# Optimization experiments

Measured on AMD Instinct MI355X. Metric: run time of the kernel, lower is better.

Reference implementation:

```python
import jax, jax.numpy as jnp
import numpy as np

B, S, D = 4, 512, 256
NEG = -1e30  # finite stand-in for -inf so fully-masked row 0 stays NaN-free


def setup_inputs() -> dict:
    key = jax.random.key(0)
    ks = jax.random.split(key, 10)
    s = 0.02
    return {
        "x": jax.random.normal(ks[0], (B, S, D), dtype=jnp.float32),
        # edge_mlp: Linear(3D -> D), ReLU, Linear(D -> 1). Stored [in, out].
        "W1": jax.random.normal(ks[1], (3 * D, D), dtype=jnp.float32) * s,
        "b1": jnp.zeros((D,), dtype=jnp.float32),
        "w2": jax.random.normal(ks[2], (D, 1), dtype=jnp.float32) * s,
        "b2": jnp.zeros((1,), dtype=jnp.float32),
        "Wv": jax.random.normal(ks[3], (D, D), dtype=jnp.float32) * s,
        "bv": jnp.zeros((D,), dtype=jnp.float32),
        "Wo": jax.random.normal(ks[4], (D, D), dtype=jnp.float32) * s,
        "bo": jnp.zeros((D,), dtype=jnp.float32),
        "gamma": jnp.ones((D,), dtype=jnp.float32),
        "beta": jnp.zeros((D,), dtype=jnp.float32),
    }


def reference(x, W1, b1, w2, b2, Wv, bv, Wo, bo, gamma, beta):
    b, seq, d = x.shape
    # edge_mlp layer1 on concat([x_i, x_j, x_i - x_j]) decomposes linearly:
    # h[b,i,j,:] = x_i @ (Wa + Wc) + x_j @ (Wb - Wc) + b1
    Wa, Wb, Wc = W1[:d], W1[d:2 * d], W1[2 * d:]
    hi = jnp.einsum('bid,dh->bih', x, Wa + Wc)          # [B,S,D]
    hj = jnp.einsum('bjd,dh->bjh', x, Wb - Wc)          # [B,S,D]
    h = jax.nn.relu(hi[:, :, None, :] + hj[:, None, :, :] + b1)  # [B,S,S,D]
    scores = jnp.einsum('bijh,h->bij', h, w2[:, 0]) + b2[0]      # [B,S,S]
    # strictly-lower-triangular causal mask (j < i)
    mask = jnp.tril(jnp.ones((seq, seq), dtype=bool), k=-1)
    scores = jnp.where(mask, scores, NEG)
    attn = jax.nn.softmax(scores, axis=-1)
    # row i=0 has no valid edges (torch yields NaN there); zero it instead
    row_valid = mask.any(axis=-1)                       # [S]
    attn = attn * row_valid[None, :, None].astype(attn.dtype)
    values = jnp.einsum('bjd,de->bje', x, Wv) + bv      # [B,S,D]
    message = jnp.einsum('bij,bjd->bid', attn, values)  # [B,S,D]
    out = jnp.einsum('bid,de->bie', message, Wo) + bo
    out = x + out
    # LayerNorm over last dim, eps=1e-5, biased variance (torch default)
    mu = jnp.mean(out, axis=-1, keepdims=True)
    var = jnp.mean(jnp.square(out - mu), axis=-1, keepdims=True)
    out = (out - mu) * jax.lax.rsqrt(var + 1e-5) * gamma + beta
    return out
```

## Files before the change

kernel.cpp:

```cpp
#include <hip/hip_runtime.h>
#include <math.h>

#define D 256
#define S 512
#define M 2048

typedef __attribute__((ext_vector_type(8))) short bf16x8;
typedef __attribute__((ext_vector_type(4))) float f32x4;

__device__ inline ushort f2bf(float f) {
    union { float f; unsigned u; } v; v.f = f;
    unsigned r = v.u + 0x7FFFu + ((v.u >> 16) & 1u);
    return (ushort)(r >> 16);
}

__global__ __launch_bounds__(256) void pack_all(
    const float* __restrict__ x, const float* __restrict__ W1,
    const float* __restrict__ Wv, const float* __restrict__ Wo,
    ushort* __restrict__ xb, ushort* __restrict__ WAt, ushort* __restrict__ WBt,
    ushort* __restrict__ Wvt, ushort* __restrict__ Wot)
{
    const int blk = blockIdx.x, t = threadIdx.x;
    if (blk < 64) {
        const int mat = blk >> 4;
        const int a0 = ((blk >> 2) & 3) * 64;
        const int b0 = (blk & 3) * 64;
        __shared__ ushort lt[64][72];
        const int r = t >> 4;
        const int c = (t & 15) * 4;
#pragma unroll
        for (int p = 0; p < 4; ++p) {
            const int sr = b0 + p * 16 + r;
            float4 v;
            if (mat == 0) {
                float4 wa = *(const float4*)(W1 + (size_t)sr * 256 + a0 + c);
                float4 wc = *(const float4*)(W1 + (size_t)(512 + sr) * 256 + a0 + c);
                v = make_float4(wa.x + wc.x, wa.y + wc.y, wa.z + wc.z, wa.w + wc.w);
            } else if (mat == 1) {
                float4 wb = *(const float4*)(W1 + (size_t)(256 + sr) * 256 + a0 + c);
                float4 wc = *(const float4*)(W1 + (size_t)(512 + sr) * 256 + a0 + c);
                v = make_float4(wb.x - wc.x, wb.y - wc.y, wb.z - wc.z, wb.w - wc.w);
            } else if (mat == 2) {
                v = *(const float4*)(Wv + (size_t)sr * 256 + a0 + c);
            } else {
                v = *(const float4*)(Wo + (size_t)sr * 256 + a0 + c);
            }
            lt[p * 16 + r][c + 0] = f2bf(v.x);
            lt[p * 16 + r][c + 1] = f2bf(v.y);
            lt[p * 16 + r][c + 2] = f2bf(v.z);
            lt[p * 16 + r][c + 3] = f2bf(v.w);
        }
        __syncthreads();
        ushort* dst = (mat == 0) ? WAt : (mat == 1) ? WBt : (mat == 2) ? Wvt : Wot;
#pragma unroll
        for (int p = 0; p < 4; ++p) {
            const int dr = p * 16 + r;
            ushort4 o = make_ushort4(lt[c + 0][dr], lt[c + 1][dr],
                                     lt[c + 2][dr], lt[c + 3][dr]);
            *(ushort4*)(dst + (size_t)(a0 + dr) * 256 + b0 + c) = o;
        }
    } else {
        const int idx = ((blk - 64) * 256 + t) * 8;
        float4 v0 = *(const float4*)(x + idx);
        float4 v1 = *(const float4*)(x + idx + 4);
        *(ushort4*)(xb + idx)     = make_ushort4(f2bf(v0.x), f2bf(v0.y), f2bf(v0.z), f2bf(v0.w));
        *(ushort4*)(xb + idx + 4) = make_ushort4(f2bf(v1.x), f2bf(v1.y), f2bf(v1.z), f2bf(v1.w));
    }
}

__global__ __launch_bounds__(256) void gemm_qkv_mfma(
    const ushort* __restrict__ xb, const ushort* __restrict__ WAt,
    const ushort* __restrict__ WBt, const ushort* __restrict__ Wvt,
    const float* __restrict__ b1, const float* __restrict__ bv,
    float* __restrict__ hi, float* __restrict__ hj, ushort* __restrict__ vals_bf)
{
    const int bn = blockIdx.x, bm = blockIdx.y;
    const int n0 = bn * 64, m0 = bm * 64;
    const int region = n0 >> 8, c0 = n0 & 255;
    const ushort* Bt = (region == 0) ? WAt : (region == 1) ? WBt : Wvt;
    const int t = threadIdx.x, w = t >> 6, l = t & 63;
    const int q = l >> 4, ln = l & 15;
    const int wm = (w >> 1) * 32, wn = (w & 1) * 32;

    f32x4 acc[2][2] = {};
    for (int k0 = 0; k0 < 256; k0 += 32) {
        bf16x8 a[2], b[2];
#pragma unroll
        for (int mt = 0; mt < 2; ++mt)
            a[mt] = *(const bf16x8*)(xb + (size_t)(m0 + wm + mt * 16 + ln) * 256 + k0 + q * 8);
#pragma unroll
        for (int nt = 0; nt < 2; ++nt)
            b[nt] = *(const bf16x8*)(Bt + (size_t)(c0 + wn + nt * 16 + ln) * 256 + k0 + q * 8);
#pragma unroll
        for (int mt = 0; mt < 2; ++mt)
#pragma unroll
            for (int nt = 0; nt < 2; ++nt)
                acc[mt][nt] = __builtin_amdgcn_mfma_f32_16x16x32_bf16(a[mt], b[nt], acc[mt][nt], 0, 0, 0);
    }

    if (region < 2) {
        float* dst = (region == 0) ? hi : hj;
#pragma unroll
        for (int nt = 0; nt < 2; ++nt) {
            const int col = c0 + wn + nt * 16 + ln;
            const float bias = (region == 0) ? b1[col] : 0.f;
#pragma unroll
            for (int mt = 0; mt < 2; ++mt)
#pragma unroll
                for (int r = 0; r < 4; ++r) {
                    const int row = m0 + wm + mt * 16 + q * 4 + r;
                    dst[(size_t)row * 256 + col] = acc[mt][nt][r] + bias;
                }
        }
    } else {
#pragma unroll
        for (int nt = 0; nt < 2; ++nt) {
            const int col = c0 + wn + nt * 16 + ln;
            const float bias = bv[col];
#pragma unroll
            for (int mt = 0; mt < 2; ++mt)
#pragma unroll
                for (int r = 0; r < 4; ++r) {
                    const int row = m0 + wm + mt * 16 + q * 4 + r;
                    vals_bf[(size_t)row * 256 + col] = f2bf(acc[mt][nt][r] + bias);
                }
        }
    }
}

__global__ __launch_bounds__(256) void scores_tiled(
    const float* __restrict__ hi, const float* __restrict__ hj,
    const float* __restrict__ w2, const float* __restrict__ b2,
    float* __restrict__ sc)
{
    const int jt = blockIdx.x, it = blockIdx.y, b = blockIdx.z;
    if (jt > it) return;
    const int i0 = it * 32, j0 = jt * 32;
    const int t = threadIdx.x;

    __shared__ __align__(16) float His[32][64];
    __shared__ __align__(16) float Hjs[32][64];
    __shared__ __align__(16) float w2s[256];

    if (t < 64) *(float4*)&w2s[t * 4] = *(const float4*)(w2 + t * 4);

    const int r = t & 31;
    const int cbase = (t >> 5) * 4;
    const float* hirow = hi + ((b << 9) + i0 + r) * D;
    const float* hjrow = hj + ((b << 9) + j0 + r) * D;

    const int ti4 = (t & 15) * 4;
    const int tj4 = (t >> 4) * 4;

    float acc00 = 0.f, acc01 = 0.f, acc10 = 0.f, acc11 = 0.f;

    for (int hc = 0; hc < 256; hc += 64) {
        const int c4a = cbase, c4b = cbase + 32;
        float4 a0 = *(const float4*)(hirow + hc + c4a);
        float4 a1 = *(const float4*)(hirow + hc + c4b);
        float4 e0 = *(const float4*)(hjrow + hc + c4a);
        float4 e1 = *(const float4*)(hjrow + hc + c4b);
        __syncthreads();
        *(float2*)&His[(c4a >> 1) + 0][2 * r] = make_float2(a0.x, a0.y);
        *(float2*)&His[(c4a >> 1) + 1][2 * r] = make_float2(a0.z, a0.w);
        *(float2*)&His[(c4b >> 1) + 0][2 * r] = make_float2(a1.x, a1.y);
        *(float2*)&His[(c4b >> 1) + 1][2 * r] = make_float2(a1.z, a1.w);
        *(float2*)&Hjs[(c4a >> 1) + 0][2 * r] = make_float2(e0.x, e0.y);
        *(float2*)&Hjs[(c4a >> 1) + 1][2 * r] = make_float2(e0.z, e0.w);
        *(float2*)&Hjs[(c4b >> 1) + 0][2 * r] = make_float2(e1.x, e1.y);
        *(float2*)&Hjs[(c4b >> 1) + 1][2 * r] = make_float2(e1.z, e1.w);
        __syncthreads();
#pragma unroll 8
        for (int h2 = 0; h2 < 32; ++h2) {
            float4 a = *(const float4*)&His[h2][ti4];
            float4 e = *(const float4*)&Hjs[h2][tj4];
            float2 w = *(const float2*)&w2s[hc + h2 * 2];
            acc00 += fmaxf(a.x + e.x, 0.f) * w.x + fmaxf(a.y + e.y, 0.f) * w.y;
            acc01 += fmaxf(a.x + e.z, 0.f) * w.x + fmaxf(a.y + e.w, 0.f) * w.y;
            acc10 += fmaxf(a.z + e.x, 0.f) * w.x + fmaxf(a.w + e.y, 0.f) * w.y;
            acc11 += fmaxf(a.z + e.z, 0.f) * w.x + fmaxf(a.w + e.w, 0.f) * w.y;
        }
    }

    const float b2v = b2[0];
    float* srow = sc + ((size_t)b << 18) + (size_t)(i0 + ((t & 15) << 1)) * S
                + j0 + ((t >> 4) << 1);
    srow[0] = acc00 + b2v;
    srow[1] = acc01 + b2v;
    srow[S] = acc10 + b2v;
    srow[S + 1] = acc11 + b2v;
}

__global__ __launch_bounds__(256) void attn_norm(
    const float* __restrict__ sc, ushort* __restrict__ attn_bf)
{
    const int row = blockIdx.x;
    const int b = row >> 9, i = row & 511;
    const int t = threadIdx.x, wave = t >> 6, lane = t & 63;
    ushort* arow = attn_bf + ((size_t)(b << 9) + i) * S;

    if (i == 0) { arow[t] = 0; arow[t + 256] = 0; return; }

    const float* srow = sc + ((size_t)b << 18) + (size_t)i * S;
    __shared__ float s[S];
    __shared__ float red[8];

    float mloc = -3.0e38f;
    for (int j = t; j < i; j += 256) { float v = srow[j]; s[j] = v; mloc = fmaxf(mloc, v); }
#pragma unroll
    for (int off = 32; off; off >>= 1) mloc = fmaxf(mloc, __shfl_xor(mloc, off, 64));
    if (lane == 0) red[wave] = mloc;
    __syncthreads();
    const float mx = fmaxf(fmaxf(red[0], red[1]), fmaxf(red[2], red[3]));

    float sloc = 0.f;
    for (int j = t; j < i; j += 256) {
        float e = __expf(s[j] - mx);
        s[j] = e;
        sloc += e;
    }
#pragma unroll
    for (int off = 32; off; off >>= 1) sloc += __shfl_xor(sloc, off, 64);
    if (lane == 0) red[4 + wave] = sloc;
    __syncthreads();
    const float inv = 1.f / (red[4] + red[5] + red[6] + red[7]);

    for (int j = t; j < S; j += 256)
        arow[j] = (j < i) ? f2bf(s[j] * inv) : (ushort)0;
}

__global__ __launch_bounds__(256) void pv_mfma(
    const ushort* __restrict__ attn_bf, const ushort* __restrict__ vals_bf,
    ushort* __restrict__ msg_bf)
{
    const int bn = blockIdx.x, bm = blockIdx.y, b = blockIdx.z;
    const int n0 = bn * 64, m0 = bm * 64;
    const ushort* A = attn_bf + ((size_t)b << 18);
    const ushort* V = vals_bf + ((size_t)(b << 9)) * 256;
    const int t = threadIdx.x, w = t >> 6, l = t & 63;
    const int q = l >> 4, ln = l & 15;
    const int wm = (w >> 1) * 32, wn = (w & 1) * 32;

    f32x4 acc[2][2] = {};
    const int kmax = m0 + 64;
    for (int k0 = 0; k0 < kmax; k0 += 32) {
        bf16x8 a[2], bb[2];
#pragma unroll
        for (int mt = 0; mt < 2; ++mt)
            a[mt] = *(const bf16x8*)(A + (size_t)(m0 + wm + mt * 16 + ln) * S + k0 + q * 8);
#pragma unroll
        for (int nt = 0; nt < 2; ++nt) {
            const int n = n0 + wn + nt * 16 + ln;
            union { bf16x8 v; short s[8]; } u;
#pragma unroll
            for (int j = 0; j < 8; ++j)
                u.s[j] = (short)V[(size_t)(k0 + q * 8 + j) * 256 + n];
            bb[nt] = u.v;
        }
#pragma unroll
        for (int mt = 0; mt < 2; ++mt)
#pragma unroll
            for (int nt = 0; nt < 2; ++nt)
                acc[mt][nt] = __builtin_amdgcn_mfma_f32_16x16x32_bf16(a[mt], bb[nt], acc[mt][nt], 0, 0, 0);
    }
#pragma unroll
    for (int nt = 0; nt < 2; ++nt) {
        const int col = n0 + wn + nt * 16 + ln;
#pragma unroll
        for (int mt = 0; mt < 2; ++mt)
#pragma unroll
            for (int r = 0; r < 4; ++r) {
                const int row = (b << 9) + m0 + wm + mt * 16 + q * 4 + r;
                msg_bf[(size_t)row * 256 + col] = f2bf(acc[mt][nt][r]);
            }
    }
}

__global__ __launch_bounds__(256) void out_ln_mfma(
    const ushort* __restrict__ msg_bf, const ushort* __restrict__ Wot,
    const float* __restrict__ x, const float* __restrict__ bo,
    const float* __restrict__ gamma, const float* __restrict__ beta,
    float* __restrict__ out)
{
    const int bm = blockIdx.x;
    const int t = threadIdx.x, w = t >> 6, l = t & 63;
    const int q = l >> 4, ln = l & 15;
    const int rbase = bm * 64 + w * 16;

    f32x4 acc[16] = {};
    for (int k0 = 0; k0 < 256; k0 += 32) {
        bf16x8 a = *(const bf16x8*)(msg_bf + (size_t)(rbase + ln) * 256 + k0 + q * 8);
#pragma unroll
        for (int nt = 0; nt < 16; ++nt) {
            bf16x8 bb = *(const bf16x8*)(Wot + (size_t)(nt * 16 + ln) * 256 + k0 + q * 8);
            acc[nt] = __builtin_amdgcn_mfma_f32_16x16x32_bf16(a, bb, acc[nt], 0, 0, 0);
        }
    }

    float sum[4] = {}, sq[4] = {};
#pragma unroll
    for (int nt = 0; nt < 16; ++nt) {
        const int col = nt * 16 + ln;
        const float bov = bo[col];
#pragma unroll
        for (int r = 0; r < 4; ++r) {
            const int row = rbase + q * 4 + r;
            float v = acc[nt][r] + x[(size_t)row * 256 + col] + bov;
            acc[nt][r] = v;
            sum[r] += v;
            sq[r] += v * v;
        }
    }
#pragma unroll
    for (int r = 0; r < 4; ++r) {
#pragma unroll
        for (int off = 1; off < 16; off <<= 1) {
            sum[r] += __shfl_xor(sum[r], off, 64);
            sq[r]  += __shfl_xor(sq[r],  off, 64);
        }
    }
#pragma unroll
    for (int nt = 0; nt < 16; ++nt) {
        const int col = nt * 16 + ln;
        const float g = gamma[col], be = beta[col];
#pragma unroll
        for (int r = 0; r < 4; ++r) {
            const float mu = sum[r] * (1.f / 256.f);
            const float var = sq[r] * (1.f / 256.f) - mu * mu;
            const int row = rbase + q * 4 + r;
            out[(size_t)row * 256 + col] =
                (acc[nt][r] - mu) * rsqrtf(var + 1e-5f) * g + be;
        }
    }
}

extern "C" void kernel_launch(void* const* d_in, const int* in_sizes, int n_in,
                              void* d_out, int out_size, void* d_ws, size_t ws_size,
                              hipStream_t stream)
{
    (void)in_sizes; (void)n_in; (void)out_size; (void)ws_size;
    const float* x     = (const float*)d_in[0];
    const float* W1    = (const float*)d_in[1];
    const float* b1    = (const float*)d_in[2];
    const float* w2    = (const float*)d_in[3];
    const float* b2    = (const float*)d_in[4];
    const float* Wv    = (const float*)d_in[5];
    const float* bv    = (const float*)d_in[6];
    const float* Wo    = (const float*)d_in[7];
    const float* bo    = (const float*)d_in[8];
    const float* gamma = (const float*)d_in[9];
    const float* beta  = (const float*)d_in[10];
    float* out = (float*)d_out;

    float* ws = (float*)d_ws;
    const size_t CH = 64 * 1024;
    float*  hi      = ws;
    float*  hj      = ws + 8 * CH;
    float*  sc      = ws + 16 * CH;
    ushort* xb      = (ushort*)(ws + 32 * CH);
    ushort* WAt     = (ushort*)(ws + 36 * CH);
    ushort* WBt     = (ushort*)(ws + 37 * CH);
    ushort* Wvt     = (ushort*)(ws + 38 * CH);
    ushort* Wot     = (ushort*)(ws + 39 * CH);
    ushort* vals_bf = (ushort*)(ws + 40 * CH);
    ushort* attn_bf = (ushort*)(ws + 44 * CH);
    ushort* msg_bf  = (ushort*)(ws + 52 * CH);

    pack_all     <<<dim3(320),        256, 0, stream>>>(x, W1, Wv, Wo, xb, WAt, WBt, Wvt, Wot);
    gemm_qkv_mfma<<<dim3(12, 32),     256, 0, stream>>>(xb, WAt, WBt, Wvt, b1, bv, hi, hj, vals_bf);
    scores_tiled <<<dim3(16, 16, 4),  256, 0, stream>>>(hi, hj, w2, b2, sc);
    attn_norm    <<<dim3(M),          256, 0, stream>>>(sc, attn_bf);
    pv_mfma      <<<dim3(4, 8, 4),    256, 0, stream>>>(attn_bf, vals_bf, msg_bf);
    out_ln_mfma  <<<dim3(32),         256, 0, stream>>>(msg_bf, Wot, x, bo, gamma, beta, out);
}
```

Baseline: 152.3 us.

## Fuse x conversion into GEMM, transpose values, retile scores and out-LN

Several changes land together. The x-to-bf16 pack moves into the QKV GEMM, which converts x on the fly, and the GEMM writes values transposed through LDS so the PV GEMM can use vector loads instead of strided gathers. The scores kernel is rewritten to use 64-row i tiles with hj held in registers per thread, and it drops the b2 add, which softmax cancels anyway. The output+LayerNorm kernel now runs 128 blocks of 16 rows, with the row reduction done across waves in shared memory. This raises parallelism and removes uncoalesced loads, at the cost of redundant x conversion in each N-tile block and more register pressure in the scores kernel.

```diff
diff --git a/kernel.cpp b/kernel.cpp
--- a/kernel.cpp
+++ b/kernel.cpp
@@ -14,65 +14,56 @@
     return (ushort)(r >> 16);
 }
 
-__global__ __launch_bounds__(256) void pack_all(
-    const float* __restrict__ x, const float* __restrict__ W1,
-    const float* __restrict__ Wv, const float* __restrict__ Wo,
-    ushort* __restrict__ xb, ushort* __restrict__ WAt, ushort* __restrict__ WBt,
-    ushort* __restrict__ Wvt, ushort* __restrict__ Wot)
+__global__ __launch_bounds__(256) void pack_w(
+    const float* __restrict__ W1, const float* __restrict__ Wv,
+    const float* __restrict__ Wo, ushort* __restrict__ WAt,
+    ushort* __restrict__ WBt, ushort* __restrict__ Wvt, ushort* __restrict__ Wot)
 {
     const int blk = blockIdx.x, t = threadIdx.x;
-    if (blk < 64) {
-        const int mat = blk >> 4;
-        const int a0 = ((blk >> 2) & 3) * 64;
-        const int b0 = (blk & 3) * 64;
-        __shared__ ushort lt[64][72];
-        const int r = t >> 4;
-        const int c = (t & 15) * 4;
-#pragma unroll
-        for (int p = 0; p < 4; ++p) {
-            const int sr = b0 + p * 16 + r;
-            float4 v;
-            if (mat == 0) {
-                float4 wa = *(const float4*)(W1 + (size_t)sr * 256 + a0 + c);
-                float4 wc = *(const float4*)(W1 + (size_t)(512 + sr) * 256 + a0 + c);
-                v = make_float4(wa.x + wc.x, wa.y + wc.y, wa.z + wc.z, wa.w + wc.w);
-            } else if (mat == 1) {
-                float4 wb = *(const float4*)(W1 + (size_t)(256 + sr) * 256 + a0 + c);
-                float4 wc = *(const float4*)(W1 + (size_t)(512 + sr) * 256 + a0 + c);
-                v = make_float4(wb.x - wc.x, wb.y - wc.y, wb.z - wc.z, wb.w - wc.w);
-            } else if (mat == 2) {
-                v = *(const float4*)(Wv + (size_t)sr * 256 + a0 + c);
-            } else {
-                v = *(const float4*)(Wo + (size_t)sr * 256 + a0 + c);
-            }
-            lt[p * 16 + r][c + 0] = f2bf(v.x);
-            lt[p * 16 + r][c + 1] = f2bf(v.y);
-            lt[p * 16 + r][c + 2] = f2bf(v.z);
-            lt[p * 16 + r][c + 3] = f2bf(v.w);
-        }
-        __syncthreads();
-        ushort* dst = (mat == 0) ? WAt : (mat == 1) ? WBt : (mat == 2) ? Wvt : Wot;
-#pragma unroll
-        for (int p = 0; p < 4; ++p) {
-            const int dr = p * 16 + r;
-            ushort4 o = make_ushort4(lt[c + 0][dr], lt[c + 1][dr],
-                                     lt[c + 2][dr], lt[c + 3][dr]);
-            *(ushort4*)(dst + (size_t)(a0 + dr) * 256 + b0 + c) = o;
-        }
-    } else {
-        const int idx = ((blk - 64) * 256 + t) * 8;
-        float4 v0 = *(const float4*)(x + idx);
-        float4 v1 = *(const float4*)(x + idx + 4);
-        *(ushort4*)(xb + idx)     = make_ushort4(f2bf(v0.x), f2bf(v0.y), f2bf(v0.z), f2bf(v0.w));
-        *(ushort4*)(xb + idx + 4) = make_ushort4(f2bf(v1.x), f2bf(v1.y), f2bf(v1.z), f2bf(v1.w));
+    const int mat = blk >> 4;
+    const int a0 = ((blk >> 2) & 3) * 64;
+    const int b0 = (blk & 3) * 64;
+    __shared__ ushort lt[64][72];
+    const int r = t >> 4;
+    const int c = (t & 15) * 4;
+#pragma unroll
+    for (int p = 0; p < 4; ++p) {
+        const int sr = b0 + p * 16 + r;
+        float4 v;
+        if (mat == 0) {
+            float4 wa = *(const float4*)(W1 + (size_t)sr * 256 + a0 + c);
+            float4 wc = *(const float4*)(W1 + (size_t)(512 + sr) * 256 + a0 + c);
+            v = make_float4(wa.x + wc.x, wa.y + wc.y, wa.z + wc.z, wa.w + wc.w);
+        } else if (mat == 1) {
+            float4 wb = *(const float4*)(W1 + (size_t)(256 + sr) * 256 + a0 + c);
+            float4 wc = *(const float4*)(W1 + (size_t)(512 + sr) * 256 + a0 + c);
+            v = make_float4(wb.x - wc.x, wb.y - wc.y, wb.z - wc.z, wb.w - wc.w);
+        } else if (mat == 2) {
+            v = *(const float4*)(Wv + (size_t)sr * 256 + a0 + c);
+        } else {
+            v = *(const float4*)(Wo + (size_t)sr * 256 + a0 + c);
+        }
+        lt[p * 16 + r][c + 0] = f2bf(v.x);
+        lt[p * 16 + r][c + 1] = f2bf(v.y);
+        lt[p * 16 + r][c + 2] = f2bf(v.z);
+        lt[p * 16 + r][c + 3] = f2bf(v.w);
+    }
+    __syncthreads();
+    ushort* dst = (mat == 0) ? WAt : (mat == 1) ? WBt : (mat == 2) ? Wvt : Wot;
+#pragma unroll
+    for (int p = 0; p < 4; ++p) {
+        const int dr = p * 16 + r;
+        ushort4 o = make_ushort4(lt[c + 0][dr], lt[c + 1][dr],
+                                 lt[c + 2][dr], lt[c + 3][dr]);
+        *(ushort4*)(dst + (size_t)(a0 + dr) * 256 + b0 + c) = o;
     }
 }
 
 __global__ __launch_bounds__(256) void gemm_qkv_mfma(
-    const ushort* __restrict__ xb, const ushort* __restrict__ WAt,
+    const float* __restrict__ x, const ushort* __restrict__ WAt,
     const ushort* __restrict__ WBt, const ushort* __restrict__ Wvt,
     const float* __restrict__ b1, const float* __restrict__ bv,
-    float* __restrict__ hi, float* __restrict__ hj, ushort* __restrict__ vals_bf)
+    float* __restrict__ hi, float* __restrict__ hj, ushort* __restrict__ vals_t)
 {
     const int bn = blockIdx.x, bm = blockIdx.y;
     const int n0 = bn * 64, m0 = bm * 64;
@@ -82,12 +73,22 @@
     const int q = l >> 4, ln = l & 15;
     const int wm = (w >> 1) * 32, wn = (w & 1) * 32;
 
+    __shared__ ushort T[64][72];
+
     f32x4 acc[2][2] = {};
     for (int k0 = 0; k0 < 256; k0 += 32) {
-        bf16x8 a[2], b[2];
-#pragma unroll
-        for (int mt = 0; mt < 2; ++mt)
-            a[mt] = *(const bf16x8*)(xb + (size_t)(m0 + wm + mt * 16 + ln) * 256 + k0 + q * 8);
+        union { bf16x8 v; ushort s[8]; } a[2];
+        bf16x8 b[2];
+#pragma unroll
+        for (int mt = 0; mt < 2; ++mt) {
+            const float* xr = x + (size_t)(m0 + wm + mt * 16 + ln) * 256 + k0 + q * 8;
+            float4 u0 = *(const float4*)xr;
+            float4 u1 = *(const float4*)(xr + 4);
+            a[mt].s[0] = f2bf(u0.x); a[mt].s[1] = f2bf(u0.y);
+            a[mt].s[2] = f2bf(u0.z); a[mt].s[3] = f2bf(u0.w);
+            a[mt].s[4] = f2bf(u1.x); a[mt].s[5] = f2bf(u1.y);
+            a[mt].s[6] = f2bf(u1.z); a[mt].s[7] = f2bf(u1.w);
+        }
 #pragma unroll
         for (int nt = 0; nt < 2; ++nt)
             b[nt] = *(const bf16x8*)(Bt + (size_t)(c0 + wn + nt * 16 + ln) * 256 + k0 + q * 8);
@@ -95,7 +96,7 @@
         for (int mt = 0; mt < 2; ++mt)
 #pragma unroll
             for (int nt = 0; nt < 2; ++nt)
-                acc[mt][nt] = __builtin_amdgcn_mfma_f32_16x16x32_bf16(a[mt], b[nt], acc[mt][nt], 0, 0, 0);
+                acc[mt][nt] = __builtin_amdgcn_mfma_f32_16x16x32_bf16(a[mt].v, b[nt], acc[mt][nt], 0, 0, 0);
     }
 
     if (region < 2) {
@@ -115,80 +116,90 @@
     } else {
 #pragma unroll
         for (int nt = 0; nt < 2; ++nt) {
-            const int col = c0 + wn + nt * 16 + ln;
-            const float bias = bv[col];
+            const int cl = wn + nt * 16 + ln;
+            const float bias = bv[c0 + cl];
 #pragma unroll
             for (int mt = 0; mt < 2; ++mt)
 #pragma unroll
-                for (int r = 0; r < 4; ++r) {
-                    const int row = m0 + wm + mt * 16 + q * 4 + r;
-                    vals_bf[(size_t)row * 256 + col] = f2bf(acc[mt][nt][r] + bias);
-                }
-        }
-    }
-}
-
-__global__ __launch_bounds__(256) void scores_tiled(
+                for (int r = 0; r < 4; ++r)
+                    T[cl][wm + mt * 16 + q * 4 + r] = f2bf(acc[mt][nt][r] + bias);
+        }
+        __syncthreads();
+        const int bb = m0 >> 9, jloc = m0 & 511;
+#pragma unroll
+        for (int p = 0; p < 2; ++p) {
+            const int idx = p * 256 + t;
+            const int e_l = idx & 63, jc = (idx >> 6) * 8;
+            *(uint4*)(vals_t + ((size_t)(bb * 256 + c0 + e_l)) * 512 + jloc + jc) =
+                *(const uint4*)&T[e_l][jc];
+        }
+    }
+}
+
+__global__ __launch_bounds__(256) void scores64(
     const float* __restrict__ hi, const float* __restrict__ hj,
-    const float* __restrict__ w2, const float* __restrict__ b2,
-    float* __restrict__ sc)
-{
-    const int jt = blockIdx.x, it = blockIdx.y, b = blockIdx.z;
-    if (jt > it) return;
-    const int i0 = it * 32, j0 = jt * 32;
-    const int t = threadIdx.x;
+    const float* __restrict__ w2, float* __restrict__ sc)
+{
+    const int jt = blockIdx.x, it = blockIdx.y, bb = blockIdx.z;
+    if (jt > 2 * it + 1) return;
+    const int i0 = it * 64, j0 = jt * 32;
+    const int t = threadIdx.x, w = t >> 6, l = t & 63;
+    const int q = l >> 4, ln = l & 15;
 
     __shared__ __align__(16) float His[32][64];
-    __shared__ __align__(16) float Hjs[32][64];
-    __shared__ __align__(16) float w2s[256];
-
+    __shared__ __align__(16) float Sst[64][36];
+    __shared__ float w2s[256];
     if (t < 64) *(float4*)&w2s[t * 4] = *(const float4*)(w2 + t * 4);
 
-    const int r = t & 31;
-    const int cbase = (t >> 5) * 4;
-    const float* hirow = hi + ((b << 9) + i0 + r) * D;
-    const float* hjrow = hj + ((b << 9) + j0 + r) * D;
-
-    const int ti4 = (t & 15) * 4;
-    const int tj4 = (t >> 4) * 4;
+    const int si = t & 63, sh = (t >> 6) * 8;
+    const float* hisrc = hi + (size_t)((bb << 9) + i0 + si) * 256 + sh;
+    const int jrow = w * 8 + q * 2;
+    const float* hj0 = hj + (size_t)((bb << 9) + j0 + jrow) * 256;
+    const float* hj1 = hj0 + 256;
 
     float acc00 = 0.f, acc01 = 0.f, acc10 = 0.f, acc11 = 0.f;
-
-    for (int hc = 0; hc < 256; hc += 64) {
-        const int c4a = cbase, c4b = cbase + 32;
-        float4 a0 = *(const float4*)(hirow + hc + c4a);
-        float4 a1 = *(const float4*)(hirow + hc + c4b);
-        float4 e0 = *(const float4*)(hjrow + hc + c4a);
-        float4 e1 = *(const float4*)(hjrow + hc + c4b);
+    float acc20 = 0.f, acc21 = 0.f, acc30 = 0.f, acc31 = 0.f;
+
+    for (int hc = 0; hc < 256; hc += 32) {
+        float4 a0 = *(const float4*)(hisrc + hc);
+        float4 a1 = *(const float4*)(hisrc + hc + 4);
+        float e0[32], e1[32];
+#pragma unroll
+        for (int c = 0; c < 8; ++c) {
+            *(float4*)&e0[c * 4] = *(const float4*)(hj0 + hc + c * 4);
+            *(float4*)&e1[c * 4] = *(const float4*)(hj1 + hc + c * 4);
+        }
         __syncthreads();
-        *(float2*)&His[(c4a >> 1) + 0][2 * r] = make_float2(a0.x, a0.y);
-        *(float2*)&His[(c4a >> 1) + 1][2 * r] = make_float2(a0.z, a0.w);
-        *(float2*)&His[(c4b >> 1) + 0][2 * r] = make_float2(a1.x, a1.y);
-        *(float2*)&His[(c4b >> 1) + 1][2 * r] = make_float2(a1.z, a1.w);
-        *(float2*)&Hjs[(c4a >> 1) + 0][2 * r] = make_float2(e0.x, e0.y);
-        *(float2*)&Hjs[(c4a >> 1) + 1][2 * r] = make_float2(e0.z, e0.w);
-        *(float2*)&Hjs[(c4b >> 1) + 0][2 * r] = make_float2(e1.x, e1.y);
-        *(float2*)&Hjs[(c4b >> 1) + 1][2 * r] = make_float2(e1.z, e1.w);
+        His[sh + 0][si] = a0.x; His[sh + 1][si] = a0.y;
+        His[sh + 2][si] = a0.z; His[sh + 3][si] = a0.w;
+        His[sh + 4][si] = a1.x; His[sh + 5][si] = a1.y;
+        His[sh + 6][si] = a1.z; His[sh + 7][si] = a1.w;
         __syncthreads();
-#pragma unroll 8
-        for (int h2 = 0; h2 < 32; ++h2) {
-            float4 a = *(const float4*)&His[h2][ti4];
-            float4 e = *(const float4*)&Hjs[h2][tj4];
-            float2 w = *(const float2*)&w2s[hc + h2 * 2];
-            acc00 += fmaxf(a.x + e.x, 0.f) * w.x + fmaxf(a.y + e.y, 0.f) * w.y;
-            acc01 += fmaxf(a.x + e.z, 0.f) * w.x + fmaxf(a.y + e.w, 0.f) * w.y;
-            acc10 += fmaxf(a.z + e.x, 0.f) * w.x + fmaxf(a.w + e.y, 0.f) * w.y;
-            acc11 += fmaxf(a.z + e.z, 0.f) * w.x + fmaxf(a.w + e.w, 0.f) * w.y;
-        }
-    }
-
-    const float b2v = b2[0];
-    float* srow = sc + ((size_t)b << 18) + (size_t)(i0 + ((t & 15) << 1)) * S
-                + j0 + ((t >> 4) << 1);
-    srow[0] = acc00 + b2v;
-    srow[1] = acc01 + b2v;
-    srow[S] = acc10 + b2v;
-    srow[S + 1] = acc11 + b2v;
+#pragma unroll
+        for (int h = 0; h < 32; ++h) {
+            float4 a = *(const float4*)&His[h][ln * 4];
+            const float wv = w2s[hc + h];
+            const float f0 = e0[h], f1 = e1[h];
+            acc00 += fmaxf(a.x + f0, 0.f) * wv;
+            acc01 += fmaxf(a.x + f1, 0.f) * wv;
+            acc10 += fmaxf(a.y + f0, 0.f) * wv;
+            acc11 += fmaxf(a.y + f1, 0.f) * wv;
+            acc20 += fmaxf(a.z + f0, 0.f) * wv;
+            acc21 += fmaxf(a.z + f1, 0.f) * wv;
+            acc30 += fmaxf(a.w + f0, 0.f) * wv;
+            acc31 += fmaxf(a.w + f1, 0.f) * wv;
+        }
+    }
+
+    Sst[ln * 4 + 0][jrow] = acc00;  Sst[ln * 4 + 0][jrow + 1] = acc01;
+    Sst[ln * 4 + 1][jrow] = acc10;  Sst[ln * 4 + 1][jrow + 1] = acc11;
+    Sst[ln * 4 + 2][jrow] = acc20;  Sst[ln * 4 + 2][jrow + 1] = acc21;
+    Sst[ln * 4 + 3][jrow] = acc30;  Sst[ln * 4 + 3][jrow + 1] = acc31;
+    __syncthreads();
+    const int i_l = t >> 2, jc = (t & 3) * 8;
+    float* dst = sc + ((size_t)bb << 18) + (size_t)(i0 + i_l) * 512 + j0 + jc;
+    *(float4*)dst       = *(const float4*)&Sst[i_l][jc];
+    *(float4*)(dst + 4) = *(const float4*)&Sst[i_l][jc + 4];
 }
 
 __global__ __launch_bounds__(256) void attn_norm(
@@ -230,13 +241,13 @@
 }
 
 __global__ __launch_bounds__(256) void pv_mfma(
-    const ushort* __restrict__ attn_bf, const ushort* __restrict__ vals_bf,
+    const ushort* __restrict__ attn_bf, const ushort* __restrict__ vals_t,
     ushort* __restrict__ msg_bf)
 {
     const int bn = blockIdx.x, bm = blockIdx.y, b = blockIdx.z;
     const int n0 = bn * 64, m0 = bm * 64;
     const ushort* A = attn_bf + ((size_t)b << 18);
-    const ushort* V = vals_bf + ((size_t)(b << 9)) * 256;
+    const ushort* V = vals_t + (size_t)(b * 256) * 512;
     const int t = threadIdx.x, w = t >> 6, l = t & 63;
     const int q = l >> 4, ln = l & 15;
     const int wm = (w >> 1) * 32, wn = (w & 1) * 32;
@@ -249,14 +260,8 @@
         for (int mt = 0; mt < 2; ++mt)
             a[mt] = *(const bf16x8*)(A + (size_t)(m0 + wm + mt * 16 + ln) * S + k0 + q * 8);
 #pragma unroll
-        for (int nt = 0; nt < 2; ++nt) {
-            const int n = n0 + wn + nt * 16 + ln;
-            union { bf16x8 v; short s[8]; } u;
-#pragma unroll
-            for (int j = 0; j < 8; ++j)
-                u.s[j] = (short)V[(size_t)(k0 + q * 8 + j) * 256 + n];
-            bb[nt] = u.v;
-        }
+        for (int nt = 0; nt < 2; ++nt)
+            bb[nt] = *(const bf16x8*)(V + (size_t)(n0 + wn + nt * 16 + ln) * 512 + k0 + q * 8);
 #pragma unroll
         for (int mt = 0; mt < 2; ++mt)
 #pragma unroll
@@ -282,29 +287,30 @@
     const float* __restrict__ gamma, const float* __restrict__ beta,
     float* __restrict__ out)
 {
-    const int bm = blockIdx.x;
+    const int r0 = blockIdx.x * 16;
     const int t = threadIdx.x, w = t >> 6, l = t & 63;
     const int q = l >> 4, ln = l & 15;
-    const int rbase = bm * 64 + w * 16;
-
-    f32x4 acc[16] = {};
+
+    __shared__ float redS[16][4], redQ[16][4];
+
+    f32x4 acc[4] = {};
     for (int k0 = 0; k0 < 256; k0 += 32) {
-        bf16x8 a = *(const bf16x8*)(msg_bf + (size_t)(rbase + ln) * 256 + k0 + q * 8);
-#pragma unroll
-        for (int nt = 0; nt < 16; ++nt) {
-            bf16x8 bb = *(const bf16x8*)(Wot + (size_t)(nt * 16 + ln) * 256 + k0 + q * 8);
+        bf16x8 a = *(const bf16x8*)(msg_bf + (size_t)(r0 + ln) * 256 + k0 + q * 8);
+#pragma unroll
+        for (int nt = 0; nt < 4; ++nt) {
+            bf16x8 bb = *(const bf16x8*)(Wot + (size_t)(w * 64 + nt * 16 + ln) * 256 + k0 + q * 8);
             acc[nt] = __builtin_amdgcn_mfma_f32_16x16x32_bf16(a, bb, acc[nt], 0, 0, 0);
         }
     }
 
     float sum[4] = {}, sq[4] = {};
 #pragma unroll
-    for (int nt = 0; nt < 16; ++nt) {
-        const int col = nt * 16 + ln;
+    for (int nt = 0; nt < 4; ++nt) {
+        const int col = w * 64 + nt * 16 + ln;
         const float bov = bo[col];
 #pragma unroll
         for (int r = 0; r < 4; ++r) {
-            const int row = rbase + q * 4 + r;
+            const int row = r0 + q * 4 + r;
             float v = acc[nt][r] + x[(size_t)row * 256 + col] + bov;
             acc[nt][r] = v;
             sum[r] += v;
@@ -319,16 +325,26 @@
             sq[r]  += __shfl_xor(sq[r],  off, 64);
         }
     }
-#pragma unroll
-    for (int nt = 0; nt < 16; ++nt) {
-        const int col = nt * 16 + ln;
+    if (ln == 0) {
+#pragma unroll
+        for (int r = 0; r < 4; ++r) {
+            redS[q * 4 + r][w] = sum[r];
+            redQ[q * 4 + r][w] = sq[r];
+        }
+    }
+    __syncthreads();
+#pragma unroll
+    for (int nt = 0; nt < 4; ++nt) {
+        const int col = w * 64 + nt * 16 + ln;
         const float g = gamma[col], be = beta[col];
 #pragma unroll
         for (int r = 0; r < 4; ++r) {
-            const float mu = sum[r] * (1.f / 256.f);
-            const float var = sq[r] * (1.f / 256.f) - mu * mu;
-            const int row = rbase + q * 4 + r;
-            out[(size_t)row * 256 + col] =
+            const int rl = q * 4 + r;
+            const float ts = redS[rl][0] + redS[rl][1] + redS[rl][2] + redS[rl][3];
+            const float tq = redQ[rl][0] + redQ[rl][1] + redQ[rl][2] + redQ[rl][3];
+            const float mu = ts * (1.f / 256.f);
+            const float var = tq * (1.f / 256.f) - mu * mu;
+            out[(size_t)(r0 + rl) * 256 + col] =
                 (acc[nt][r] - mu) * rsqrtf(var + 1e-5f) * g + be;
         }
     }
@@ -343,7 +359,6 @@
     const float* W1    = (const float*)d_in[1];
     const float* b1    = (const float*)d_in[2];
     const float* w2    = (const float*)d_in[3];
-    const float* b2    = (const float*)d_in[4];
     const float* Wv    = (const float*)d_in[5];
     const float* bv    = (const float*)d_in[6];
     const float* Wo    = (const float*)d_in[7];
@@ -357,19 +372,18 @@
     float*  hi      = ws;
     float*  hj      = ws + 8 * CH;
     float*  sc      = ws + 16 * CH;
-    ushort* xb      = (ushort*)(ws + 32 * CH);
-    ushort* WAt     = (ushort*)(ws + 36 * CH);
-    ushort* WBt     = (ushort*)(ws + 37 * CH);
-    ushort* Wvt     = (ushort*)(ws + 38 * CH);
-    ushort* Wot     = (ushort*)(ws + 39 * CH);
-    ushort* vals_bf = (ushort*)(ws + 40 * CH);
-    ushort* attn_bf = (ushort*)(ws + 44 * CH);
-    ushort* msg_bf  = (ushort*)(ws + 52 * CH);
-
-    pack_all     <<<dim3(320),        256, 0, stream>>>(x, W1, Wv, Wo, xb, WAt, WBt, Wvt, Wot);
-    gemm_qkv_mfma<<<dim3(12, 32),     256, 0, stream>>>(xb, WAt, WBt, Wvt, b1, bv, hi, hj, vals_bf);
-    scores_tiled <<<dim3(16, 16, 4),  256, 0, stream>>>(hi, hj, w2, b2, sc);
-    attn_norm    <<<dim3(M),          256, 0, stream>>>(sc, attn_bf);
-    pv_mfma      <<<dim3(4, 8, 4),    256, 0, stream>>>(attn_bf, vals_bf, msg_bf);
-    out_ln_mfma  <<<dim3(32),         256, 0, stream>>>(msg_bf, Wot, x, bo, gamma, beta, out);
-}
+    ushort* WAt     = (ushort*)(ws + 32 * CH);
+    ushort* WBt     = (ushort*)(ws + 33 * CH);
+    ushort* Wvt     = (ushort*)(ws + 34 * CH);
+    ushort* Wot     = (ushort*)(ws + 35 * CH);
+    ushort* vals_t  = (ushort*)(ws + 36 * CH);
+    ushort* attn_bf = (ushort*)(ws + 40 * CH);
+    ushort* msg_bf  = (ushort*)(ws + 48 * CH);
+
+    pack_w       <<<dim3(64),        256, 0, stream>>>(W1, Wv, Wo, WAt, WBt, Wvt, Wot);
+    gemm_qkv_mfma<<<dim3(12, 32),    256, 0, stream>>>(x, WAt, WBt, Wvt, b1, bv, hi, hj, vals_t);
+    scores64     <<<dim3(16, 8, 4),  256, 0, stream>>>(hi, hj, w2, sc);
+    attn_norm    <<<dim3(M),         256, 0, stream>>>(sc, attn_bf);
+    pv_mfma      <<<dim3(4, 8, 4),   256, 0, stream>>>(attn_bf, vals_t, msg_bf);
+    out_ln_mfma  <<<dim3(128),       256, 0, stream>>>(msg_bf, Wot, x, bo, gamma, beta, out);
+}
```

Measured after the change: 141.0 us. -7.4%, faster.
